# Optimization experiments

Hardware: AMD Instinct MI355X
Metric: run time of the kernel (lower is better)

## Reference

```python
import jax, jax.numpy as jnp
import numpy as np

LAM = 0.003  # kernel_lam squash threshold


def setup_inputs() -> dict:
    key = jax.random.key(0)
    k1, k2, k3, k4 = jax.random.split(key, 4)
    B, L, H, Lk = 2, 4096, 2048, 128
    u = jax.random.normal(k1, (B, L, H), jnp.float32)
    # LongConvKernel parameter [channels=1, H, Lk]; scaled so squash keeps most taps nonzero
    kernel = jax.random.normal(k2, (1, H, Lk), jnp.float32) * 0.05
    D = jax.random.normal(k3, (1, H), jnp.float32)  # skip term [channels, H]
    # output_linear: nn.Linear(H, 2H) followed by GLU(dim=-1)
    W = jax.random.normal(k4, (2 * H, H), jnp.float32) / np.sqrt(H)
    b = jnp.zeros((2 * H,), jnp.float32)
    return {"u": u, "kernel": kernel, "D": D, "W": W, "b": b}


def reference(u, kernel, D, W, b):
    # u: [B, L, H] -> transpose to [B, H, L]
    B, L, H = u.shape
    ut = jnp.transpose(u, (0, 2, 1)).astype(jnp.float32)  # bhl
    # LongConvKernel forward: squash k = relu(|k| - lam) * sign(k)
    k = jnp.maximum(jnp.abs(kernel) - LAM, 0.0) * jnp.sign(kernel)  # [C, H, Lk]
    Lk = kernel.shape[-1]
    n = Lk + L  # FFT size for linear (causal) convolution
    k_f = jnp.fft.rfft(k, n=n)          # [C, H, n//2+1]
    u_f = jnp.fft.rfft(ut, n=n)         # [B, H, n//2+1]
    y_f = jnp.einsum('bhl,chl->bchl', u_f, k_f)
    y = jnp.fft.irfft(y_f, n=n)[..., :L]  # [B, C, H, L]
    # source adds the D skip term twice (duplicated line) -> factor 2
    y = y + 2.0 * jnp.einsum('bhl,ch->bchl', ut, D)
    # rearrange 'b c h l -> b (c h) l' then transpose -> [B, L, C*H]
    y = jnp.transpose(y.reshape(B, -1, L), (0, 2, 1))
    y = jax.nn.gelu(y, approximate=False)  # torch GELU is exact erf
    z = y @ W.T + b                     # [B, L, 2H]
    a, g = jnp.split(z, 2, axis=-1)     # GLU along last dim
    return a * jax.nn.sigmoid(g)        # [B, L, H]
```

## Files before the change

kernel.cpp:

```cpp
#include <hip/hip_runtime.h>
#include <hip/hip_bf16.h>
#include <cstdint>

constexpr int Bc  = 2;
constexpr int Lc  = 4096;
constexpr int Hc  = 2048;
constexpr int LKc = 128;
constexpr float LAMc = 0.003f;

typedef __attribute__((ext_vector_type(8))) __bf16 bf16x8;
typedef __attribute__((ext_vector_type(4))) float  f32x4;

__device__ __forceinline__ void gl_lds16(const void* g, void* lds) {
  __builtin_amdgcn_global_load_lds(
      (const __attribute__((address_space(1))) uint32_t*)(uintptr_t)g,
      (__attribute__((address_space(3))) uint32_t*)(uint32_t)(uintptr_t)lds,
      16, 0, 0);
}

__global__ __launch_bounds__(256) void squash_kernel(
    const float* __restrict__ kin, float* __restrict__ kq) {
  const int idx = blockIdx.x * 256 + threadIdx.x;
  const int j = idx >> 11;
  const int h = idx & (Hc - 1);
  const float v = kin[h * LKc + j];
  const float a = fabsf(v) - LAMc;
  kq[idx] = (a > 0.f) ? copysignf(a, v) : 0.f;
}

__global__ __launch_bounds__(256) void wcast_kernel(
    const float* __restrict__ W, __hip_bfloat16* __restrict__ Wb) {
  const int idx = (blockIdx.x * 256 + threadIdx.x) * 4;
  const float4 v = *(const float4*)(W + idx);
  Wb[idx + 0] = __float2bfloat16(v.x);
  Wb[idx + 1] = __float2bfloat16(v.y);
  Wb[idx + 2] = __float2bfloat16(v.z);
  Wb[idx + 3] = __float2bfloat16(v.w);
}

template <bool CHECK>
__device__ __forceinline__ void conv_accum(
    const float* __restrict__ ub, const float* __restrict__ kq,
    const int h, const int l0, float acc[16], float win[23]) {
#pragma unroll
  for (int x = 0; x < 23; ++x) {
    const int il = l0 - 127 + x;
    win[x] = (!CHECK || il >= 0) ? ub[(size_t)il * Hc] : 0.f;
  }
#pragma unroll 4
  for (int c = 0; c < 15; ++c) {
    float t[8];
#pragma unroll
    for (int d = 0; d < 8; ++d) t[d] = kq[(127 - 8 * c - d) * Hc + h];
#pragma unroll
    for (int d = 0; d < 8; ++d)
#pragma unroll
      for (int i = 0; i < 16; ++i)
        acc[i] = fmaf(t[d], win[i + d], acc[i]);
#pragma unroll
    for (int x = 0; x < 15; ++x) win[x] = win[x + 8];
#pragma unroll
    for (int x = 15; x < 23; ++x) {
      const int il = l0 - 127 + 8 * (c + 1) + x;
      win[x] = (!CHECK || il >= 0) ? ub[(size_t)il * Hc] : 0.f;
    }
  }
  {
    float t[8];
#pragma unroll
    for (int d = 0; d < 8; ++d) t[d] = kq[(7 - d) * Hc + h];
#pragma unroll
    for (int d = 0; d < 8; ++d)
#pragma unroll
      for (int i = 0; i < 16; ++i)
        acc[i] = fmaf(t[d], win[i + d], acc[i]);
  }
}

__global__ __launch_bounds__(256) void conv_gelu_kernel(
    const float* __restrict__ u, const float* __restrict__ kq,
    const float* __restrict__ Dp, __hip_bfloat16* __restrict__ Aout) {
  const int lane = threadIdx.x & 63;
  const int wv   = threadIdx.x >> 6;
  const int h  = blockIdx.y * 64 + lane;
  const int l0 = blockIdx.x * 64 + wv * 16;
  const int b  = blockIdx.z;
  const float* ub = u + (size_t)b * Lc * Hc + h;

  float acc[16], win[23];
#pragma unroll
  for (int i = 0; i < 16; ++i) acc[i] = 0.f;

  if (blockIdx.x >= 2)
    conv_accum<false>(ub, kq, h, l0, acc, win);
  else
    conv_accum<true>(ub, kq, h, l0, acc, win);

  const float dv = 2.f * Dp[h];
  const size_t obase = ((size_t)b * Lc + l0) * (size_t)Hc + h;
#pragma unroll
  for (int i = 0; i < 16; ++i) {
    const float y  = fmaf(dv, win[i + 7], acc[i]);
    const float ge = 0.5f * y * (1.f + erff(y * 0.70710678118654752f));
    Aout[obase + (size_t)i * Hc] = __float2bfloat16(ge);
  }
}

__global__ __launch_bounds__(256, 2) void gemm_glu_kernel(
    const __hip_bfloat16* __restrict__ A, const __hip_bfloat16* __restrict__ Wb,
    const float* __restrict__ bias, float* __restrict__ out) {
  __shared__ __align__(16) __hip_bfloat16 As[128 * 32];
  __shared__ __align__(16) __hip_bfloat16 Bs[128 * 32];

  const int t    = threadIdx.x;
  const int lane = t & 63;
  const int wv   = t >> 6;
  const int quad = lane >> 4;
  const int l16  = lane & 15;
  const int m0 = blockIdx.x * 128;
  const int n0 = blockIdx.y * 64;

  f32x4 accA[2][4], accG[2][4];
#pragma unroll
  for (int i = 0; i < 2; ++i)
#pragma unroll
    for (int j = 0; j < 4; ++j) {
      accA[i][j] = f32x4{0.f, 0.f, 0.f, 0.f};
      accG[i][j] = f32x4{0.f, 0.f, 0.f, 0.f};
    }

  const int srow = t >> 2;
  const int scol = (t & 3) * 8;
  const __hip_bfloat16* gA0 = A  + (size_t)(m0 + srow) * Hc + scol;
  const __hip_bfloat16* gA1 = A  + (size_t)(m0 + 64 + srow) * Hc + scol;
  const __hip_bfloat16* gBa = Wb + (size_t)(n0 + srow) * Hc + scol;
  const __hip_bfloat16* gBg = Wb + (size_t)(Hc + n0 + srow) * Hc + scol;
  char* ldsA0 = (char*)As + wv * 1024;
  char* ldsA1 = (char*)As + 4096 + wv * 1024;
  char* ldsBa = (char*)Bs + wv * 1024;
  char* ldsBg = (char*)Bs + 4096 + wv * 1024;

  const bf16x8* ar0 = (const bf16x8*)(As + (wv * 32 + l16) * 32 + quad * 8);
  const bf16x8* ar1 = (const bf16x8*)(As + (wv * 32 + 16 + l16) * 32 + quad * 8);

  for (int it = 0; it < 64; ++it) {
    const int k0 = it * 32;
    gl_lds16(gA0 + k0, ldsA0);
    gl_lds16(gA1 + k0, ldsA1);
    gl_lds16(gBa + k0, ldsBa);
    gl_lds16(gBg + k0, ldsBg);
    __syncthreads();
    const bf16x8 af0 = *ar0;
    const bf16x8 af1 = *ar1;
#pragma unroll
    for (int nj = 0; nj < 4; ++nj) {
      const bf16x8 ba = *(const bf16x8*)(Bs + (nj * 16 + l16) * 32 + quad * 8);
      const bf16x8 bg = *(const bf16x8*)(Bs + (64 + nj * 16 + l16) * 32 + quad * 8);
      accA[0][nj] = __builtin_amdgcn_mfma_f32_16x16x32_bf16(af0, ba, accA[0][nj], 0, 0, 0);
      accA[1][nj] = __builtin_amdgcn_mfma_f32_16x16x32_bf16(af1, ba, accA[1][nj], 0, 0, 0);
      accG[0][nj] = __builtin_amdgcn_mfma_f32_16x16x32_bf16(af0, bg, accG[0][nj], 0, 0, 0);
      accG[1][nj] = __builtin_amdgcn_mfma_f32_16x16x32_bf16(af1, bg, accG[1][nj], 0, 0, 0);
    }
    __syncthreads();
  }

  const int mbase = m0 + wv * 32;
#pragma unroll
  for (int mi = 0; mi < 2; ++mi) {
#pragma unroll
    for (int nj = 0; nj < 4; ++nj) {
      const int n = n0 + nj * 16 + l16;
      const float ba_ = bias[n];
      const float bg_ = bias[Hc + n];
#pragma unroll
      for (int r = 0; r < 4; ++r) {
        const int m = mbase + mi * 16 + quad * 4 + r;
        const float a = accA[mi][nj][r] + ba_;
        const float g = accG[mi][nj][r] + bg_;
        out[(size_t)m * Hc + n] = a * (1.f / (1.f + expf(-g)));
      }
    }
  }
}

extern "C" void kernel_launch(void* const* d_in, const int* in_sizes, int n_in,
                              void* d_out, int out_size, void* d_ws, size_t ws_size,
                              hipStream_t stream) {
  const float* u    = (const float*)d_in[0];
  const float* kin  = (const float*)d_in[1];
  const float* Dp   = (const float*)d_in[2];
  const float* W    = (const float*)d_in[3];
  const float* bias = (const float*)d_in[4];
  float* out = (float*)d_out;

  char* ws = (char*)d_ws;
  float*          kq = (float*)ws;
  __hip_bfloat16* Wb = (__hip_bfloat16*)(ws + (1 << 20));
  __hip_bfloat16* Am = (__hip_bfloat16*)(ws + (17 << 20));

  squash_kernel<<<(Hc * LKc) / 256, 256, 0, stream>>>(kin, kq);
  wcast_kernel<<<(2 * Hc * Hc) / 1024, 256, 0, stream>>>(W, Wb);
  conv_gelu_kernel<<<dim3(Lc / 64, Hc / 64, Bc), 256, 0, stream>>>(u, kq, Dp, Am);
  gemm_glu_kernel<<<dim3((Bc * Lc) / 128, Hc / 64), 256, 0, stream>>>(Am, Wb, bias, out);
}
```

Baseline: 393.1 us.

## Vectorize conv over two channels, swizzle GEMM LDS, use fast exp

The direct convolution now has each thread handle two adjacent channels with float2 loads and packed FMAs, halving the grid in H, fully unrolling the tap loop and storing bf16 pairs. The GEMM applies an XOR swizzle to the LDS tile layout, on both the global-to-LDS copy and the fragment reads, to reduce bank conflicts. The sigmoid uses __expf instead of expf. The goals are wider memory transactions, packed FP32 math and fewer LDS conflicts, at the cost of more registers per conv thread (possibly lower occupancy) and slightly less accurate exp.

```diff
diff --git a/kernel.cpp b/kernel.cpp
--- a/kernel.cpp
+++ b/kernel.cpp
@@ -10,6 +10,7 @@
 
 typedef __attribute__((ext_vector_type(8))) __bf16 bf16x8;
 typedef __attribute__((ext_vector_type(4))) float  f32x4;
+typedef __attribute__((ext_vector_type(2))) float  f32x2;
 
 __device__ __forceinline__ void gl_lds16(const void* g, void* lds) {
   __builtin_amdgcn_global_load_lds(
@@ -39,41 +40,44 @@
 }
 
 template <bool CHECK>
-__device__ __forceinline__ void conv_accum(
-    const float* __restrict__ ub, const float* __restrict__ kq,
-    const int h, const int l0, float acc[16], float win[23]) {
+__device__ __forceinline__ void conv_accum2(
+    const float* __restrict__ ub, const float* __restrict__ kqh,
+    const int l0, f32x2 acc[16], f32x2 win[23]) {
 #pragma unroll
   for (int x = 0; x < 23; ++x) {
     const int il = l0 - 127 + x;
-    win[x] = (!CHECK || il >= 0) ? ub[(size_t)il * Hc] : 0.f;
-  }
-#pragma unroll 4
+    win[x] = (!CHECK || il >= 0) ? *(const f32x2*)(ub + (size_t)il * Hc)
+                                 : f32x2{0.f, 0.f};
+  }
+#pragma unroll
   for (int c = 0; c < 15; ++c) {
-    float t[8];
-#pragma unroll
-    for (int d = 0; d < 8; ++d) t[d] = kq[(127 - 8 * c - d) * Hc + h];
+    f32x2 t[8];
 #pragma unroll
     for (int d = 0; d < 8; ++d)
+      t[d] = *(const f32x2*)(kqh + (127 - 8 * c - d) * Hc);
+#pragma unroll
+    for (int d = 0; d < 8; ++d)
 #pragma unroll
       for (int i = 0; i < 16; ++i)
-        acc[i] = fmaf(t[d], win[i + d], acc[i]);
+        acc[i] = __builtin_elementwise_fma(t[d], win[i + d], acc[i]);
 #pragma unroll
     for (int x = 0; x < 15; ++x) win[x] = win[x + 8];
 #pragma unroll
     for (int x = 15; x < 23; ++x) {
       const int il = l0 - 127 + 8 * (c + 1) + x;
-      win[x] = (!CHECK || il >= 0) ? ub[(size_t)il * Hc] : 0.f;
+      win[x] = (!CHECK || il >= 0) ? *(const f32x2*)(ub + (size_t)il * Hc)
+                                   : f32x2{0.f, 0.f};
     }
   }
   {
-    float t[8];
-#pragma unroll
-    for (int d = 0; d < 8; ++d) t[d] = kq[(7 - d) * Hc + h];
+    f32x2 t[8];
+#pragma unroll
+    for (int d = 0; d < 8; ++d) t[d] = *(const f32x2*)(kqh + (7 - d) * Hc);
 #pragma unroll
     for (int d = 0; d < 8; ++d)
 #pragma unroll
       for (int i = 0; i < 16; ++i)
-        acc[i] = fmaf(t[d], win[i + d], acc[i]);
+        acc[i] = __builtin_elementwise_fma(t[d], win[i + d], acc[i]);
   }
 }
 
@@ -82,28 +86,39 @@
     const float* __restrict__ Dp, __hip_bfloat16* __restrict__ Aout) {
   const int lane = threadIdx.x & 63;
   const int wv   = threadIdx.x >> 6;
-  const int h  = blockIdx.y * 64 + lane;
+  const int h  = blockIdx.y * 128 + lane * 2;
   const int l0 = blockIdx.x * 64 + wv * 16;
   const int b  = blockIdx.z;
-  const float* ub = u + (size_t)b * Lc * Hc + h;
-
-  float acc[16], win[23];
-#pragma unroll
-  for (int i = 0; i < 16; ++i) acc[i] = 0.f;
+  const float* ub  = u + (size_t)b * Lc * Hc + h;
+  const float* kqh = kq + h;
+
+  f32x2 acc[16], win[23];
+#pragma unroll
+  for (int i = 0; i < 16; ++i) acc[i] = f32x2{0.f, 0.f};
 
   if (blockIdx.x >= 2)
-    conv_accum<false>(ub, kq, h, l0, acc, win);
+    conv_accum2<false>(ub, kqh, l0, acc, win);
   else
-    conv_accum<true>(ub, kq, h, l0, acc, win);
-
-  const float dv = 2.f * Dp[h];
+    conv_accum2<true>(ub, kqh, l0, acc, win);
+
+  const f32x2 d2 = *(const f32x2*)(Dp + h);
+  const f32x2 dv = f32x2{2.f * d2.x, 2.f * d2.y};
   const size_t obase = ((size_t)b * Lc + l0) * (size_t)Hc + h;
 #pragma unroll
   for (int i = 0; i < 16; ++i) {
-    const float y  = fmaf(dv, win[i + 7], acc[i]);
-    const float ge = 0.5f * y * (1.f + erff(y * 0.70710678118654752f));
-    Aout[obase + (size_t)i * Hc] = __float2bfloat16(ge);
-  }
+    const f32x2 y = __builtin_elementwise_fma(dv, win[i + 7], acc[i]);
+    const float gx = 0.5f * y.x * (1.f + erff(y.x * 0.70710678118654752f));
+    const float gy = 0.5f * y.y * (1.f + erff(y.y * 0.70710678118654752f));
+    __hip_bfloat162 o;
+    o.x = __float2bfloat16(gx);
+    o.y = __float2bfloat16(gy);
+    *(__hip_bfloat162*)(Aout + obase + (size_t)i * Hc) = o;
+  }
+}
+
+__device__ __forceinline__ const bf16x8* frag_ptr(
+    const __hip_bfloat16* base, int r, int g) {
+  return (const bf16x8*)(base + r * 32 + ((g ^ ((r >> 1) & 3)) * 8));
 }
 
 __global__ __launch_bounds__(256, 2) void gemm_glu_kernel(
@@ -130,7 +145,8 @@
     }
 
   const int srow = t >> 2;
-  const int scol = (t & 3) * 8;
+  const int gg   = (t & 3) ^ ((srow >> 1) & 3);
+  const int scol = gg * 8;
   const __hip_bfloat16* gA0 = A  + (size_t)(m0 + srow) * Hc + scol;
   const __hip_bfloat16* gA1 = A  + (size_t)(m0 + 64 + srow) * Hc + scol;
   const __hip_bfloat16* gBa = Wb + (size_t)(n0 + srow) * Hc + scol;
@@ -140,8 +156,8 @@
   char* ldsBa = (char*)Bs + wv * 1024;
   char* ldsBg = (char*)Bs + 4096 + wv * 1024;
 
-  const bf16x8* ar0 = (const bf16x8*)(As + (wv * 32 + l16) * 32 + quad * 8);
-  const bf16x8* ar1 = (const bf16x8*)(As + (wv * 32 + 16 + l16) * 32 + quad * 8);
+  const bf16x8* ar0 = frag_ptr(As, wv * 32 + l16, quad);
+  const bf16x8* ar1 = frag_ptr(As, wv * 32 + 16 + l16, quad);
 
   for (int it = 0; it < 64; ++it) {
     const int k0 = it * 32;
@@ -154,8 +170,8 @@
     const bf16x8 af1 = *ar1;
 #pragma unroll
     for (int nj = 0; nj < 4; ++nj) {
-      const bf16x8 ba = *(const bf16x8*)(Bs + (nj * 16 + l16) * 32 + quad * 8);
-      const bf16x8 bg = *(const bf16x8*)(Bs + (64 + nj * 16 + l16) * 32 + quad * 8);
+      const bf16x8 ba = *frag_ptr(Bs, nj * 16 + l16, quad);
+      const bf16x8 bg = *frag_ptr(Bs, 64 + nj * 16 + l16, quad);
       accA[0][nj] = __builtin_amdgcn_mfma_f32_16x16x32_bf16(af0, ba, accA[0][nj], 0, 0, 0);
       accA[1][nj] = __builtin_amdgcn_mfma_f32_16x16x32_bf16(af1, ba, accA[1][nj], 0, 0, 0);
       accG[0][nj] = __builtin_amdgcn_mfma_f32_16x16x32_bf16(af0, bg, accG[0][nj], 0, 0, 0);
@@ -177,7 +193,7 @@
         const int m = mbase + mi * 16 + quad * 4 + r;
         const float a = accA[mi][nj][r] + ba_;
         const float g = accG[mi][nj][r] + bg_;
-        out[(size_t)m * Hc + n] = a * (1.f / (1.f + expf(-g)));
+        out[(size_t)m * Hc + n] = a * (1.f / (1.f + __expf(-g)));
       }
     }
   }
@@ -200,6 +216,6 @@
 
   squash_kernel<<<(Hc * LKc) / 256, 256, 0, stream>>>(kin, kq);
   wcast_kernel<<<(2 * Hc * Hc) / 1024, 256, 0, stream>>>(W, Wb);
-  conv_gelu_kernel<<<dim3(Lc / 64, Hc / 64, Bc), 256, 0, stream>>>(u, kq, Dp, Am);
+  conv_gelu_kernel<<<dim3(Lc / 64, Hc / 128, Bc), 256, 0, stream>>>(u, kq, Dp, Am);
   gemm_glu_kernel<<<dim3((Bc * Lc) / 128, Hc / 64), 256, 0, stream>>>(Am, Wb, bias, out);
 }
```

Measured after the change: 471.2 us. 19.9% more time.
